# Kernel optimization log

Hardware: AMD Instinct MI355X
Metric: run time of the kernel (lower is better)

The kernel has to match this reference:

```python
import jax, jax.numpy as jnp
import numpy as np

B, N, D = 8, 2048, 768
LN_EPS = 1e-5


def setup_inputs() -> dict:
    key = jax.random.key(0)
    ks = jax.random.split(key, 5)
    scale = 1.0 / np.sqrt(D)
    features = jax.random.normal(ks[0], (B, N, D), dtype=jnp.float32)
    mask = jax.random.randint(ks[1], (B, N), 0, 2) == 1  # True = masked (padding)
    Wq = jax.random.normal(ks[2], (D, D), dtype=jnp.float32) * scale
    Wk = jax.random.normal(ks[3], (D, D), dtype=jnp.float32) * scale
    Wv = jax.random.normal(ks[4], (D, D), dtype=jnp.float32) * scale
    ln_gamma = jnp.ones((D,), dtype=jnp.float32)
    ln_beta = jnp.zeros((D,), dtype=jnp.float32)
    return {"features": features, "mask": mask, "Wq": Wq, "Wk": Wk, "Wv": Wv,
            "ln_gamma": ln_gamma, "ln_beta": ln_beta}


def reference(features, mask, Wq, Wk, Wv, ln_gamma, ln_beta):
    # LayerNorm over last dim
    mu = jnp.mean(features, axis=-1, keepdims=True)
    var = jnp.mean(jnp.square(features - mu), axis=-1, keepdims=True)
    x = (features - mu) * jax.lax.rsqrt(var + LN_EPS) * ln_gamma + ln_beta
    # torch Linear: y = x @ W.T
    Q = jnp.einsum('bnd,ed->bne', x, Wq)
    K = jnp.einsum('bnd,ed->bne', x, Wk)
    V = jnp.einsum('bnd,ed->bne', x, Wv)
    scale = x.shape[-1] ** -0.5
    scores = jnp.einsum('bnd,bmd->bnm', Q, K) * scale  # [B,N,N]
    scores = jnp.where(mask[:, None, :], -jnp.inf, scores)
    probs = jax.nn.softmax(scores, axis=-1)
    ctx = jnp.einsum('bnm,bmd->bnd', probs, V)
    return ctx
```

## Files before the change

### kernel.cpp

```cpp
#include <hip/hip_runtime.h>
#include <hip/hip_bf16.h>
#include <cstdint>

typedef __attribute__((ext_vector_type(8))) __bf16 bf16v8;
typedef __attribute__((ext_vector_type(4))) float f32x4;
typedef __attribute__((ext_vector_type(4))) unsigned short ushort4v;
typedef __attribute__((ext_vector_type(8))) unsigned short ushort8v;

#define BB 8
#define NN 2048
#define DD 768

__device__ __forceinline__ float b2f(unsigned short u) {
  union { unsigned int i; float f; } c; c.i = ((unsigned int)u) << 16; return c.f;
}
__device__ __forceinline__ unsigned short f2b(float f) {
  union { float f; unsigned int i; } c; c.f = f;
  unsigned int u = c.i;
  return (unsigned short)((u + 0x7fffu + ((u >> 16) & 1u)) >> 16);
}

__global__ __launch_bounds__(256) void ln_kernel(const float* __restrict__ x,
                                                 const float* __restrict__ gamma,
                                                 const float* __restrict__ beta,
                                                 unsigned short* __restrict__ xb) {
  int row = blockIdx.x;
  const float* xr = x + (size_t)row * DD;
  int t = threadIdx.x;
  float a0 = xr[t], a1 = xr[t + 256], a2 = xr[t + 512];
  float s = a0 + a1 + a2;
  float q = a0 * a0 + a1 * a1 + a2 * a2;
  for (int o = 32; o > 0; o >>= 1) { s += __shfl_xor(s, o); q += __shfl_xor(q, o); }
  __shared__ float red[2][4];
  int w = t >> 6, lane = t & 63;
  if (lane == 0) { red[0][w] = s; red[1][w] = q; }
  __syncthreads();
  s = red[0][0] + red[0][1] + red[0][2] + red[0][3];
  q = red[1][0] + red[1][1] + red[1][2] + red[1][3];
  float mean = s * (1.0f / DD);
  float var = q * (1.0f / DD) - mean * mean;
  float inv = rsqrtf(var + 1e-5f);
  unsigned short* o0 = xb + (size_t)row * DD;
  o0[t]       = f2b((a0 - mean) * inv * gamma[t]       + beta[t]);
  o0[t + 256] = f2b((a1 - mean) * inv * gamma[t + 256] + beta[t + 256]);
  o0[t + 512] = f2b((a2 - mean) * inv * gamma[t + 512] + beta[t + 512]);
}

__global__ __launch_bounds__(256) void wconvert(const float* __restrict__ Wq,
                                                const float* __restrict__ Wk,
                                                const float* __restrict__ Wv,
                                                unsigned short* __restrict__ Wcat) {
  int i = blockIdx.x * 256 + threadIdx.x;
  const int dd = DD * DD;
  if (i >= 3 * dd) return;
  float v;
  if (i < dd)           v = Wq[i] * 0.03608439182435161f;
  else if (i < 2 * dd)  v = Wk[i - dd];
  else                  v = Wv[i - 2 * dd];
  Wcat[i] = f2b(v);
}

__device__ __forceinline__ void gload_lds16(const void* g, void* l) {
  __builtin_amdgcn_global_load_lds(
      (const __attribute__((address_space(1))) void*)g,
      (__attribute__((address_space(3))) void*)(unsigned)(uintptr_t)l,
      16, 0, 0);
}

#define RDA(i0, ks, B)                                                                   \
  _Pragma("unroll")                                                                      \
  for (int i_ = 0; i_ < 4; ++i_)                                                         \
    aq[i_] = *(const bf16v8*)&smem[(B) + (ks) * 8192 + arow0 + ((i0) + i_) * 512 + kg8];
#define RDB(ks, B)                                                                       \
  _Pragma("unroll")                                                                      \
  for (int j_ = 0; j_ < NJ; ++j_)                                                        \
    bq[j_] = *(const bf16v8*)&smem[(B) + 16384 + (ks) * 8192 + brow0 + j_ * 512 + kg8];
#define MFQ(i0)                                                                          \
  _Pragma("unroll")                                                                      \
  for (int i_ = 0; i_ < 4; ++i_) {                                                       \
    _Pragma("unroll")                                                                    \
    for (int j_ = 0; j_ < NJ; ++j_)                                                      \
      acc[(i0) + i_][j_] = __builtin_amdgcn_mfma_f32_16x16x32_bf16(                      \
          aq[i_], bq[j_], acc[(i0) + i_][j_], 0, 0, 0);                                  \
  }
#define BARF asm volatile("s_barrier" ::: "memory")
#define VMC6 asm volatile("s_waitcnt vmcnt(6)" ::: "memory")
#define VMC0 asm volatile("s_waitcnt vmcnt(0)" ::: "memory")
#define P1   __builtin_amdgcn_s_setprio(1)
#define P0   __builtin_amdgcn_s_setprio(0)

#define TILEK(KT, CURB, NXTB)                                                            \
  do {                                                                                   \
                                                   \
    RDA(0, 0, CURB); RDB(0, CURB);                                                       \
    if ((KT) + 1 < NT) stgA((KT) + 1, 1, (NXTB));                                        \
    BARF; P1; MFQ(0); P0; BARF;                                                          \
                                       \
    RDA(4, 0, CURB);                                                                     \
    if ((KT) + 1 < NT) stgB((KT) + 1, 1, (NXTB));                                        \
    BARF; P1; MFQ(4); P0;                                                                \
    VMC6; BARF;                                                                          \
                                                   \
    RDA(0, 1, CURB); RDB(1, CURB);                                                       \
    if ((KT) + 2 < NT) stgA((KT) + 2, 0, (CURB));                                        \
    BARF; P1; MFQ(0); P0; BARF;                                                          \
                                                   \
    RDA(4, 1, CURB);                                                                     \
    if ((KT) + 2 < NT) stgB((KT) + 2, 0, (CURB));                                        \
    BARF; P1; MFQ(4); P0;                                                                \
    if ((KT) < NT - 2) { VMC6; } else { VMC0; }                                          \
    BARF;                                                                                \
  } while (0)

template <int MODE, int NJ>
__global__ __launch_bounds__(512, 2) void gemm256(
    const unsigned short* __restrict__ A, const unsigned short* __restrict__ Bm,
    unsigned short* __restrict__ Cq, unsigned short* __restrict__ Ck,
    unsigned short* __restrict__ Cv, float* __restrict__ Cf,
    int K, int lda, int ldb,
    long aStride, long bStride, long cStride) {
  extern __shared__ unsigned short smem[];
  const int BN = NJ * 64;

  const int t = threadIdx.x;
  int bx = blockIdx.x, by = blockIdx.y, bz = blockIdx.z;
  {
    const int gx = gridDim.x, gy = gridDim.y;
    const int nwg = gx * gy * (int)gridDim.z;
    int id = bx + gx * (by + gy * bz);
    int sw = (id & 7) * (nwg >> 3) + (id >> 3);
    bx = sw % gx; int r2 = sw / gx;
    by = r2 % gy; bz = r2 / gy;
  }
  const int n0 = bx * BN, m0 = by * 256;
  const unsigned short* Ab = A + (size_t)bz * aStride;
  const unsigned short* Bb = Bm + (size_t)bz * bStride;

  const int lane = t & 63;
  const int w = t >> 6;
  const int wm = w >> 2, wn = w & 3;
  const int frow = lane & 15;
  const int kg8 = (lane >> 4) * 8;
  const int arow0 = (wm * 128 + frow) * 32;
  const int brow0 = (wn * (NJ * 16) + frow) * 32;

  const unsigned short* Asrc = Ab + (size_t)(m0 + (t >> 2)) * lda + (t & 3) * 8;
  const unsigned short* Bsrc = Bb + (size_t)(n0 + (t >> 2)) * ldb + (t & 3) * 8;
  const int sdst = w * 512;

  auto stgA = [&](int kt, int ks, int bufb) {
    const unsigned short* s = Asrc + kt * 64 + ks * 32;
    gload_lds16(s, &smem[bufb + ks * 8192 + sdst]);
    gload_lds16(s + (size_t)128 * lda, &smem[bufb + ks * 8192 + 4096 + sdst]);
  };
  auto stgB = [&](int kt, int ks, int bufb) {
    const unsigned short* s = Bsrc + kt * 64 + ks * 32;
    gload_lds16(s, &smem[bufb + 16384 + ks * 8192 + sdst]);
    gload_lds16(s + (size_t)128 * ldb, &smem[bufb + 16384 + ks * 8192 + 4096 + sdst]);
  };

  f32x4 acc[8][NJ] = {};
  const int NT = K >> 6;
  bf16v8 aq[4], bq[NJ];

  stgA(0, 0, 0);     stgB(0, 0, 0);
  stgA(0, 1, 0);     stgB(0, 1, 0);
  stgA(1, 0, 32768); stgB(1, 0, 32768);
  asm volatile("s_waitcnt vmcnt(8)" ::: "memory");
  BARF;

  for (int ktp = 0; ktp < NT; ktp += 2) {
    TILEK(ktp, 0, 32768);
    TILEK(ktp + 1, 32768, 0);
  }

  const int r0 = (lane >> 4) * 4;
  const int c0 = lane & 15;
  const int mrowB = m0 + wm * 128 + r0;
  const int ncolB = n0 + wn * (NJ * 16) + c0;

  if (MODE == 0) {
    if (n0 < 1536) {
      unsigned short* dst = (n0 < 768) ? Cq : Ck;
      const int cb = (n0 < 768) ? 0 : 768;
#pragma unroll
      for (int i = 0; i < 8; ++i)
#pragma unroll
        for (int j = 0; j < NJ; ++j)
#pragma unroll
          for (int r = 0; r < 4; ++r)
            dst[(size_t)(mrowB + i * 16 + r) * DD + (ncolB + j * 16 - cb)] = f2b(acc[i][j][r]);
    } else {
#pragma unroll
      for (int i = 0; i < 8; ++i) {
        int row = mrowB + i * 16;
        int bb = row >> 11, nn = row & 2047;
#pragma unroll
        for (int j = 0; j < NJ; ++j) {
          int e = ncolB + j * 16 - 1536;
          ushort4v pk;
#pragma unroll
          for (int r = 0; r < 4; ++r) pk[r] = f2b(acc[i][j][r]);
          *(ushort4v*)&Cv[((size_t)(bb * DD + e)) * NN + nn] = pk;
        }
      }
    }
  } else if (MODE == 1) {
    unsigned short* dst = Cq + (size_t)bz * cStride;
#pragma unroll
    for (int i = 0; i < 8; ++i)
#pragma unroll
      for (int j = 0; j < NJ; ++j)
#pragma unroll
        for (int r = 0; r < 4; ++r)
          dst[(size_t)(mrowB + i * 16 + r) * NN + (ncolB + j * 16)] = f2b(acc[i][j][r]);
  } else {
    float* dst = Cf + (size_t)bz * cStride;
#pragma unroll
    for (int i = 0; i < 8; ++i)
#pragma unroll
      for (int j = 0; j < NJ; ++j)
#pragma unroll
        for (int r = 0; r < 4; ++r)
          dst[(size_t)(mrowB + i * 16 + r) * DD + (ncolB + j * 16)] = acc[i][j][r];
  }
}

__global__ __launch_bounds__(256) void softmax_mask(unsigned short* __restrict__ S,
                                                    const int* __restrict__ mask) {
  int row = blockIdx.x;
  int bb = row >> 11;
  unsigned short* sr = S + (size_t)row * NN;
  const int* mr = mask + bb * NN;
  int t = threadIdx.x;

  ushort8v pk = *(const ushort8v*)&sr[t * 8];
  float v[8];
  int msk[8];
#pragma unroll
  for (int j = 0; j < 8; ++j) msk[j] = mr[t * 8 + j];
  float mx = -1e30f;
#pragma unroll
  for (int j = 0; j < 8; ++j) {
    v[j] = b2f(pk[j]);
    if (!msk[j]) mx = fmaxf(mx, v[j]);
  }
  for (int o = 32; o > 0; o >>= 1) mx = fmaxf(mx, __shfl_xor(mx, o));
  __shared__ float redm[4], reds[4];
  int w = t >> 6, lane = t & 63;
  if (lane == 0) redm[w] = mx;
  __syncthreads();
  mx = fmaxf(fmaxf(redm[0], redm[1]), fmaxf(redm[2], redm[3]));

  float e[8];
  float sum = 0.f;
#pragma unroll
  for (int j = 0; j < 8; ++j) {
    e[j] = msk[j] ? 0.f : __expf(v[j] - mx);
    sum += e[j];
  }
  for (int o = 32; o > 0; o >>= 1) sum += __shfl_xor(sum, o);
  if (lane == 0) reds[w] = sum;
  __syncthreads();
  sum = reds[0] + reds[1] + reds[2] + reds[3];
  float inv = 1.0f / sum;

  ushort8v op;
#pragma unroll
  for (int j = 0; j < 8; ++j) op[j] = f2b(e[j] * inv);
  *(ushort8v*)&sr[t * 8] = op;
}

extern "C" void kernel_launch(void* const* d_in, const int* in_sizes, int n_in,
                              void* d_out, int out_size, void* d_ws, size_t ws_size,
                              hipStream_t stream) {
  const float* features = (const float*)d_in[0];
  const int* mask       = (const int*)d_in[1];
  const float* Wq       = (const float*)d_in[2];
  const float* Wk       = (const float*)d_in[3];
  const float* Wv       = (const float*)d_in[4];
  const float* gamma    = (const float*)d_in[5];
  const float* beta     = (const float*)d_in[6];
  float* out = (float*)d_out;

  char* ws = (char*)d_ws;
  size_t off = 0;
  auto alloc = [&](size_t bytes) {
    char* p = ws + off;
    off += (bytes + 255) & ~(size_t)255;
    return p;
  };
  unsigned short* Wcat = (unsigned short*)alloc((size_t)(2304 + 64) * DD * 2);
  unsigned short* Qb   = (unsigned short*)alloc((size_t)BB * NN * DD * 2);
  unsigned short* Kb   = (unsigned short*)alloc((size_t)BB * NN * DD * 2);
  unsigned short* Vt   = (unsigned short*)alloc(((size_t)BB * DD + 64) * NN * 2);
  char* last = alloc((size_t)BB * NN * NN * 2);
  unsigned short* Sb = (unsigned short*)last;
  unsigned short* Xb = (unsigned short*)last;

  (void)hipFuncSetAttribute(reinterpret_cast<const void*>(&gemm256<0, 3>),
                            hipFuncAttributeMaxDynamicSharedMemorySize, 131072);
  (void)hipFuncSetAttribute(reinterpret_cast<const void*>(&gemm256<1, 4>),
                            hipFuncAttributeMaxDynamicSharedMemorySize, 131072);
  (void)hipFuncSetAttribute(reinterpret_cast<const void*>(&gemm256<2, 3>),
                            hipFuncAttributeMaxDynamicSharedMemorySize, 131072);

  ln_kernel<<<BB * NN, 256, 0, stream>>>(features, gamma, beta, Xb);
  wconvert<<<(3 * DD * DD + 255) / 256, 256, 0, stream>>>(Wq, Wk, Wv, Wcat);

  gemm256<0, 3><<<dim3(2304 / 192, (BB * NN) / 256, 1), 512, 131072, stream>>>(
      Xb, Wcat, Qb, Kb, Vt, nullptr, DD, DD, DD, 0, 0, 0);

  gemm256<1, 4><<<dim3(NN / 256, NN / 256, BB), 512, 131072, stream>>>(
      Qb, Kb, Sb, nullptr, nullptr, nullptr, DD, DD, DD,
      (long)NN * DD, (long)NN * DD, (long)NN * NN);

  softmax_mask<<<BB * NN, 256, 0, stream>>>(Sb, mask);

  gemm256<2, 3><<<dim3(DD / 192, NN / 256, BB), 512, 131072, stream>>>(
      Sb, Vt, nullptr, nullptr, nullptr, out, NN, NN, NN,
      (long)NN * NN, (long)DD * NN, (long)NN * DD);
}
```

Before: 241.5 us.

## Compact unmasked keys and values to skip masked columns in attention GEMMs

Adds a per-batch prefix scan over the mask. The QKV projection epilogue then scatters K and V rows for unmasked tokens into compacted buffers, and the padding is zero-filled up to tile multiples. The QK^T GEMM exits early for column tiles past the compacted count, softmax only reads and writes the live columns, and the PV GEMM shortens its K loop to the rounded live count. This cuts roughly half the score and PV work for a random mask, at the cost of extra small kernels and scalar scattered stores in the projection epilogue.

```diff
diff --git a/kernel.cpp b/kernel.cpp
--- a/kernel.cpp
+++ b/kernel.cpp
@@ -60,6 +60,49 @@
   Wcat[i] = f2b(v);
 }
 
+__global__ __launch_bounds__(256) void mask_scan(const int* __restrict__ mask,
+                                                 int* __restrict__ pfx,
+                                                 int* __restrict__ ncnt) {
+  int b = blockIdx.x;
+  const int* mr = mask + b * NN;
+  int t = threadIdx.x;
+  int v[8]; int s = 0;
+#pragma unroll
+  for (int j = 0; j < 8; ++j) { v[j] = (mr[t * 8 + j] == 0) ? 1 : 0; s += v[j]; }
+  int lane = t & 63, w = t >> 6;
+  int x = s;
+  for (int o = 1; o < 64; o <<= 1) { int y = __shfl_up(x, o); if (lane >= o) x += y; }
+  __shared__ int wsum[4];
+  if (lane == 63) wsum[w] = x;
+  __syncthreads();
+  int base = 0;
+#pragma unroll
+  for (int i = 0; i < 4; ++i) if (i < w) base += wsum[i];
+  int run = base + x - s;
+#pragma unroll
+  for (int j = 0; j < 8; ++j) { pfx[b * NN + t * 8 + j] = run; run += v[j]; }
+  if (t == 255) ncnt[b] = base + x;
+}
+
+__global__ __launch_bounds__(256) void padzero(const int* __restrict__ ncnt,
+                                               unsigned short* __restrict__ Kc,
+                                               unsigned short* __restrict__ Vtc) {
+  int b = blockIdx.x & 7, sub = blockIdx.x >> 3;
+  int nc = ncnt[b];
+  int r256 = (nc + 255) & ~255, r128 = (nc + 127) & ~127;
+  int cnt1 = (r256 - nc) * DD;
+  unsigned short* k0 = Kc + ((size_t)b * NN + nc) * DD;
+  for (int i = sub * 256 + threadIdx.x; i < cnt1; i += 2048) k0[i] = 0;
+  int wcols = r128 - nc;
+  if (wcols > 0) {
+    int cnt2 = DD * wcols;
+    for (int i = sub * 256 + threadIdx.x; i < cnt2; i += 2048) {
+      int e = i / wcols, c = i - e * wcols;
+      Vtc[((size_t)b * DD + e) * NN + nc + c] = 0;
+    }
+  }
+}
+
 __device__ __forceinline__ void gload_lds16(const void* g, void* l) {
   __builtin_amdgcn_global_load_lds(
       (const __attribute__((address_space(1))) void*)g,
@@ -91,20 +134,16 @@
 
 #define TILEK(KT, CURB, NXTB)                                                            \
   do {                                                                                   \
-                                                   \
     RDA(0, 0, CURB); RDB(0, CURB);                                                       \
     if ((KT) + 1 < NT) stgA((KT) + 1, 1, (NXTB));                                        \
     BARF; P1; MFQ(0); P0; BARF;                                                          \
-                                       \
     RDA(4, 0, CURB);                                                                     \
     if ((KT) + 1 < NT) stgB((KT) + 1, 1, (NXTB));                                        \
     BARF; P1; MFQ(4); P0;                                                                \
     VMC6; BARF;                                                                          \
-                                                   \
     RDA(0, 1, CURB); RDB(1, CURB);                                                       \
     if ((KT) + 2 < NT) stgA((KT) + 2, 0, (CURB));                                        \
     BARF; P1; MFQ(0); P0; BARF;                                                          \
-                                                   \
     RDA(4, 1, CURB);                                                                     \
     if ((KT) + 2 < NT) stgB((KT) + 2, 0, (CURB));                                        \
     BARF; P1; MFQ(4); P0;                                                                \
@@ -118,7 +157,9 @@
     unsigned short* __restrict__ Cq, unsigned short* __restrict__ Ck,
     unsigned short* __restrict__ Cv, float* __restrict__ Cf,
     int K, int lda, int ldb,
-    long aStride, long bStride, long cStride) {
+    long aStride, long bStride, long cStride,
+    const int* __restrict__ pfx, const int* __restrict__ msk,
+    const int* __restrict__ ncnt) {
   extern __shared__ unsigned short smem[];
   const int BN = NJ * 64;
 
@@ -133,6 +174,13 @@
     by = r2 % gy; bz = r2 / gy;
   }
   const int n0 = bx * BN, m0 = by * 256;
+
+  if (MODE == 1) {
+    const int bound = (ncnt[bz] + 255) & ~255;
+    if (n0 >= bound) return;
+  }
+  const int NT = (MODE == 2) ? (((ncnt[bz] + 127) >> 7) << 1) : (K >> 6);
+
   const unsigned short* Ab = A + (size_t)bz * aStride;
   const unsigned short* Bb = Bm + (size_t)bz * bStride;
 
@@ -144,8 +192,10 @@
   const int arow0 = (wm * 128 + frow) * 32;
   const int brow0 = (wn * (NJ * 16) + frow) * 32;
 
-  const unsigned short* Asrc = Ab + (size_t)(m0 + (t >> 2)) * lda + (t & 3) * 8;
-  const unsigned short* Bsrc = Bb + (size_t)(n0 + (t >> 2)) * ldb + (t & 3) * 8;
+  const int srow = t >> 2;
+  const int scol8 = (t & 3) * 8;
+  const unsigned short* Asrc = Ab + (size_t)(m0 + srow) * lda + scol8;
+  const unsigned short* Bsrc = Bb + (size_t)(n0 + srow) * ldb + scol8;
   const int sdst = w * 512;
 
   auto stgA = [&](int kt, int ks, int bufb) {
@@ -160,7 +210,6 @@
   };
 
   f32x4 acc[8][NJ] = {};
-  const int NT = K >> 6;
   bf16v8 aq[4], bq[NJ];
 
   stgA(0, 0, 0);     stgB(0, 0, 0);
@@ -180,28 +229,43 @@
   const int ncolB = n0 + wn * (NJ * 16) + c0;
 
   if (MODE == 0) {
-    if (n0 < 1536) {
-      unsigned short* dst = (n0 < 768) ? Cq : Ck;
-      const int cb = (n0 < 768) ? 0 : 768;
+    if (n0 < 768) {
 #pragma unroll
       for (int i = 0; i < 8; ++i)
 #pragma unroll
         for (int j = 0; j < NJ; ++j)
 #pragma unroll
           for (int r = 0; r < 4; ++r)
-            dst[(size_t)(mrowB + i * 16 + r) * DD + (ncolB + j * 16 - cb)] = f2b(acc[i][j][r]);
+            Cq[(size_t)(mrowB + i * 16 + r) * DD + (ncolB + j * 16)] = f2b(acc[i][j][r]);
+    } else if (n0 < 1536) {
+#pragma unroll
+      for (int i = 0; i < 8; ++i)
+#pragma unroll
+        for (int r = 0; r < 4; ++r) {
+          const int row = mrowB + i * 16 + r;
+          if (msk[row] == 0) {
+            const int bbb = row >> 11;
+            unsigned short* dst = Ck + ((size_t)bbb * NN + pfx[row]) * DD + (ncolB - 768);
+#pragma unroll
+            for (int j = 0; j < NJ; ++j) dst[j * 16] = f2b(acc[i][j][r]);
+          }
+        }
     } else {
 #pragma unroll
       for (int i = 0; i < 8; ++i) {
-        int row = mrowB + i * 16;
-        int bb = row >> 11, nn = row & 2047;
-#pragma unroll
-        for (int j = 0; j < NJ; ++j) {
-          int e = ncolB + j * 16 - 1536;
-          ushort4v pk;
-#pragma unroll
-          for (int r = 0; r < 4; ++r) pk[r] = f2b(acc[i][j][r]);
-          *(ushort4v*)&Cv[((size_t)(bb * DD + e)) * NN + nn] = pk;
+        const int row0 = mrowB + i * 16;
+        const int bbb = row0 >> 11;
+#pragma unroll
+        for (int r = 0; r < 4; ++r) {
+          const int tok = row0 + r;
+          if (msk[tok] == 0) {
+            const int cc = pfx[tok];
+#pragma unroll
+            for (int j = 0; j < NJ; ++j) {
+              const int e = ncolB + j * 16 - 1536;
+              Cv[((size_t)bbb * DD + e) * NN + cc] = f2b(acc[i][j][r]);
+            }
+          }
         }
       }
     }
@@ -226,24 +290,25 @@
   }
 }
 
-__global__ __launch_bounds__(256) void softmax_mask(unsigned short* __restrict__ S,
-                                                    const int* __restrict__ mask) {
+__global__ __launch_bounds__(256) void softmax_c(unsigned short* __restrict__ S,
+                                                 const int* __restrict__ ncnt) {
   int row = blockIdx.x;
   int bb = row >> 11;
+  const int nc = ncnt[bb];
+  const int p128 = (nc + 127) & ~127;
   unsigned short* sr = S + (size_t)row * NN;
-  const int* mr = mask + bb * NN;
   int t = threadIdx.x;
-
-  ushort8v pk = *(const ushort8v*)&sr[t * 8];
+  const int cbase = t * 8;
+
   float v[8];
-  int msk[8];
-#pragma unroll
-  for (int j = 0; j < 8; ++j) msk[j] = mr[t * 8 + j];
+  const bool anyload = cbase < nc;
+  ushort8v pk;
+  if (anyload) pk = *(const ushort8v*)&sr[cbase];
   float mx = -1e30f;
 #pragma unroll
   for (int j = 0; j < 8; ++j) {
-    v[j] = b2f(pk[j]);
-    if (!msk[j]) mx = fmaxf(mx, v[j]);
+    v[j] = anyload ? b2f(pk[j]) : 0.f;
+    if (cbase + j < nc) mx = fmaxf(mx, v[j]);
   }
   for (int o = 32; o > 0; o >>= 1) mx = fmaxf(mx, __shfl_xor(mx, o));
   __shared__ float redm[4], reds[4];
@@ -256,7 +321,7 @@
   float sum = 0.f;
 #pragma unroll
   for (int j = 0; j < 8; ++j) {
-    e[j] = msk[j] ? 0.f : __expf(v[j] - mx);
+    e[j] = (cbase + j < nc) ? __expf(v[j] - mx) : 0.f;
     sum += e[j];
   }
   for (int o = 32; o > 0; o >>= 1) sum += __shfl_xor(sum, o);
@@ -265,10 +330,12 @@
   sum = reds[0] + reds[1] + reds[2] + reds[3];
   float inv = 1.0f / sum;
 
-  ushort8v op;
-#pragma unroll
-  for (int j = 0; j < 8; ++j) op[j] = f2b(e[j] * inv);
-  *(ushort8v*)&sr[t * 8] = op;
+  if (cbase < p128) {
+    ushort8v op;
+#pragma unroll
+    for (int j = 0; j < 8; ++j) op[j] = f2b(e[j] * inv);
+    *(ushort8v*)&sr[cbase] = op;
+  }
 }
 
 extern "C" void kernel_launch(void* const* d_in, const int* in_sizes, int n_in,
@@ -292,8 +359,10 @@
   };
   unsigned short* Wcat = (unsigned short*)alloc((size_t)(2304 + 64) * DD * 2);
   unsigned short* Qb   = (unsigned short*)alloc((size_t)BB * NN * DD * 2);
-  unsigned short* Kb   = (unsigned short*)alloc((size_t)BB * NN * DD * 2);
-  unsigned short* Vt   = (unsigned short*)alloc(((size_t)BB * DD + 64) * NN * 2);
+  unsigned short* Kc   = (unsigned short*)alloc((size_t)BB * NN * DD * 2);
+  unsigned short* Vtc  = (unsigned short*)alloc(((size_t)BB * DD + 64) * NN * 2);
+  int* pfx  = (int*)alloc((size_t)BB * NN * 4);
+  int* ncnt = (int*)alloc(64 * 4);
   char* last = alloc((size_t)BB * NN * NN * 2);
   unsigned short* Sb = (unsigned short*)last;
   unsigned short* Xb = (unsigned short*)last;
@@ -307,17 +376,20 @@
 
   ln_kernel<<<BB * NN, 256, 0, stream>>>(features, gamma, beta, Xb);
   wconvert<<<(3 * DD * DD + 255) / 256, 256, 0, stream>>>(Wq, Wk, Wv, Wcat);
+  mask_scan<<<BB, 256, 0, stream>>>(mask, pfx, ncnt);
 
   gemm256<0, 3><<<dim3(2304 / 192, (BB * NN) / 256, 1), 512, 131072, stream>>>(
-      Xb, Wcat, Qb, Kb, Vt, nullptr, DD, DD, DD, 0, 0, 0);
+      Xb, Wcat, Qb, Kc, Vtc, nullptr, DD, DD, DD, 0, 0, 0, pfx, mask, ncnt);
+
+  padzero<<<64, 256, 0, stream>>>(ncnt, Kc, Vtc);
 
   gemm256<1, 4><<<dim3(NN / 256, NN / 256, BB), 512, 131072, stream>>>(
-      Qb, Kb, Sb, nullptr, nullptr, nullptr, DD, DD, DD,
-      (long)NN * DD, (long)NN * DD, (long)NN * NN);
-
-  softmax_mask<<<BB * NN, 256, 0, stream>>>(Sb, mask);
+      Qb, Kc, Sb, nullptr, nullptr, nullptr, DD, DD, DD,
+      (long)NN * DD, (long)NN * DD, (long)NN * NN, nullptr, nullptr, ncnt);
+
+  softmax_c<<<BB * NN, 256, 0, stream>>>(Sb, ncnt);
 
   gemm256<2, 3><<<dim3(DD / 192, NN / 256, BB), 512, 131072, stream>>>(
-      Sb, Vt, nullptr, nullptr, nullptr, out, NN, NN, NN,
-      (long)NN * NN, (long)DD * NN, (long)NN * DD);
-}
+      Sb, Vtc, nullptr, nullptr, nullptr, out, NN, NN, NN,
+      (long)NN * NN, (long)DD * NN, (long)NN * DD, nullptr, nullptr, ncnt);
+}
```

After: 247.6 us. 1.03x slower.
